# Kernel optimization log

Hardware: AMD Instinct MI355X
Metric: run time of the kernel (lower is better)

Reference implementation:

```python
import jax, jax.numpy as jnp
import numpy as np

WEIGHT = 0.1  # HISCLoss weight


def _gram(X):
    # linear kernel (the module's 'rbf' branch computes X @ Y.T)
    X = X.reshape(X.shape[0], -1)
    return X @ X.T  # [B, B]


def _center(K):
    # H K H with H = I - 11^T/B  ==  K - rowmean - colmean + grandmean
    rm = K.mean(axis=1, keepdims=True)
    cm = K.mean(axis=0, keepdims=True)
    gm = K.mean()
    return K - rm - cm + gm


def _hsic(X, Y):
    B = X.shape[0]
    Kc = _center(_gram(X))
    Lc = _center(_gram(Y))
    # trace(Kc @ Lc) without the B^3 matmul
    tr = jnp.einsum('ij,ji->', Kc, Lc)
    return tr / ((B - 1) ** 2)


def setup_inputs() -> dict:
    key = jax.random.key(0)
    ks = jax.random.split(key, 4)
    B, d = 4096, 256
    return {
        'e0': jax.random.normal(ks[0], (B, d), dtype=jnp.float32),
        'e1': jax.random.normal(ks[1], (B, d), dtype=jnp.float32),
        'e2': jax.random.normal(ks[2], (B, d), dtype=jnp.float32),
        'e3': jax.random.normal(ks[3], (B, d), dtype=jnp.float32),
    }


def reference(e0, e1, e2, e3):
    experts = [e0, e1, e2, e3]
    n = len(experts)
    vals = []
    for i in range(n):
        for j in range(i + 1, n):
            vals.append(_hsic(experts[i], experts[j]))
    L_hsic = jnp.mean(jnp.stack(vals))
    return WEIGHT * L_hsic
```

## Files before the change

### kernel.cpp

```cpp
#include <hip/hip_runtime.h>
#include <hip/hip_bf16.h>

#define B_ROWS 4096
#define DIM 256
#define NPAIR 6
#define PITCH 4160
#define BK 256
#define APITCH 264
#define KSPLIT 8
#define KCHUNK (B_ROWS / KSPLIT)

typedef short bf16x8 __attribute__((ext_vector_type(8)));
typedef float f32x4 __attribute__((ext_vector_type(4)));

__device__ __forceinline__ const float* sel(const float* e0, const float* e1,
                                            const float* e2, const float* e3, int i) {
    return i == 0 ? e0 : (i == 1 ? e1 : (i == 2 ? e2 : e3));
}

__device__ __forceinline__ int pair_i(int p) { return p < 3 ? 0 : (p < 5 ? 1 : 2); }
__device__ __forceinline__ int pair_j(int p) { return p < 3 ? p + 1 : (p < 5 ? p - 1 : 3); }

__device__ __forceinline__ unsigned short f32_to_bf16_rne(float f) {
    unsigned int u = __float_as_uint(f);
    unsigned int r = (u + 0x7FFFu + ((u >> 16) & 1u)) >> 16;
    return (unsigned short)r;
}


__global__ __launch_bounds__(256) void transpose_bf16_kernel(
        const float* __restrict__ e0, const float* __restrict__ e1,
        const float* __restrict__ e2, const float* __restrict__ e3,
        unsigned short* __restrict__ XT, float* __restrict__ sums) {
    int rt = blockIdx.x;
    int ct = blockIdx.y;
    int e  = blockIdx.z;
    const float* X = sel(e0, e1, e2, e3, e);
    unsigned short* XTe = XT + (size_t)e * DIM * PITCH;

    __shared__ float T[64][65];

    int t = threadIdx.x;
    int c4 = (t & 15) << 2;
    #pragma unroll
    for (int p = 0; p < 4; ++p) {
        int r = (t >> 4) + 16 * p;
        float4 v = *(const float4*)&X[(size_t)(rt * 64 + r) * DIM + ct * 64 + c4];
        T[c4 + 0][r] = v.x;
        T[c4 + 1][r] = v.y;
        T[c4 + 2][r] = v.z;
        T[c4 + 3][r] = v.w;
    }
    __syncthreads();

    #pragma unroll
    for (int p = 0; p < 2; ++p) {
        int id = 256 * p + t;
        int c = id >> 3;
        int roff = (id & 7) * 8;
        bf16x8 outv;
        float s8 = 0.f;
        #pragma unroll
        for (int s = 0; s < 8; ++s) {
            float f = T[c][roff + s];
            outv[s] = (short)f32_to_bf16_rne(f);
            s8 += f;
        }
        *(bf16x8*)&XTe[(size_t)(ct * 64 + c) * PITCH + rt * 64 + roff] = outv;
        s8 += __shfl_down(s8, 4, 8);
        s8 += __shfl_down(s8, 2, 8);
        s8 += __shfl_down(s8, 1, 8);
        if ((id & 7) == 0) atomicAdd(&sums[e * DIM + ct * 64 + c], s8);
    }
}

__global__ __launch_bounds__(512) void gram_v3_kernel(
        const unsigned short* __restrict__ XT, const float* __restrict__ sums,
        float* __restrict__ acc_out) {
    __shared__ __align__(16) unsigned short smem[2 * 32 * APITCH];
    unsigned short* As = smem;
    unsigned short* Bs = smem + 32 * APITCH;
    float* red = (float*)smem;

    int blk = blockIdx.x;
    int p = blk >> 6;
    int tile = blk & 63;
    int a0 = (tile >> 3) * 32;
    int b0 = (tile & 7) * 32;
    int pi = pair_i(p), pj = pair_j(p);
    const unsigned short* Xp = XT + (size_t)pi * DIM * PITCH;
    const unsigned short* Yp = XT + (size_t)pj * DIM * PITCH;

    int tid = threadIdx.x;
    int w = tid >> 6;
    int L = tid & 63;

    int srow = tid >> 5;
    int soff = (tid & 31) * 8;
    const unsigned short* gA0 = Xp + (size_t)(a0 + srow) * PITCH + soff;
    const unsigned short* gA1 = Xp + (size_t)(a0 + 16 + srow) * PITCH + soff;
    const unsigned short* gB0 = Yp + (size_t)(b0 + srow) * PITCH + soff;
    const unsigned short* gB1 = Yp + (size_t)(b0 + 16 + srow) * PITCH + soff;
    int lA0 = srow * APITCH + soff;
    int lA1 = (16 + srow) * APITCH + soff;

    bf16x8 ra0 = *(const bf16x8*)gA0;
    bf16x8 ra1 = *(const bf16x8*)gA1;
    bf16x8 rb0 = *(const bf16x8*)gB0;
    bf16x8 rb1 = *(const bf16x8*)gB1;

    f32x4 acc[2][2] = {};
    int koff = w * 32 + (L >> 4) * 8;
    int frA0 = (L & 15) * APITCH + koff;
    int frA1 = (16 + (L & 15)) * APITCH + koff;

    for (int c = 0; c < 16; ++c) {
        __syncthreads();
        *(bf16x8*)&As[lA0] = ra0;
        *(bf16x8*)&As[lA1] = ra1;
        *(bf16x8*)&Bs[lA0] = rb0;
        *(bf16x8*)&Bs[lA1] = rb1;
        int cn = (c < 15) ? (c + 1) * BK : 0;
        ra0 = *(const bf16x8*)(gA0 + cn);
        ra1 = *(const bf16x8*)(gA1 + cn);
        rb0 = *(const bf16x8*)(gB0 + cn);
        rb1 = *(const bf16x8*)(gB1 + cn);
        __syncthreads();
        bf16x8 a0f = *(const bf16x8*)&As[frA0];
        bf16x8 a1f = *(const bf16x8*)&As[frA1];
        bf16x8 b0f = *(const bf16x8*)&Bs[frA0];
        bf16x8 b1f = *(const bf16x8*)&Bs[frA1];
        acc[0][0] = __builtin_amdgcn_mfma_f32_16x16x32_bf16(a0f, b0f, acc[0][0], 0, 0, 0);
        acc[0][1] = __builtin_amdgcn_mfma_f32_16x16x32_bf16(a0f, b1f, acc[0][1], 0, 0, 0);
        acc[1][0] = __builtin_amdgcn_mfma_f32_16x16x32_bf16(a1f, b0f, acc[1][0], 0, 0, 0);
        acc[1][1] = __builtin_amdgcn_mfma_f32_16x16x32_bf16(a1f, b1f, acc[1][1], 0, 0, 0);
    }

    __syncthreads();

    #pragma unroll
    for (int ti = 0; ti < 2; ++ti)
        #pragma unroll
        for (int tj = 0; tj < 2; ++tj)
            #pragma unroll
            for (int r = 0; r < 4; ++r) {
                int m = ti * 16 + (L >> 4) * 4 + r;
                int n = tj * 16 + (L & 15);
                red[w * 1056 + m * 33 + n] = acc[ti][tj][r];
            }
    __syncthreads();

    const float inv_b = 1.0f / (float)B_ROWS;
    float local = 0.f;
    #pragma unroll
    for (int q = 0; q < 2; ++q) {
        int pos = tid + q * 512;
        int m = pos >> 5, n = pos & 31;
        float s = 0.f;
        #pragma unroll
        for (int ww = 0; ww < 8; ++ww) s += red[ww * 1056 + m * 33 + n];
        float v = s - sums[pi * DIM + a0 + m] * sums[pj * DIM + b0 + n] * inv_b;
        local = fmaf(v, v, local);
    }
    #pragma unroll
    for (int off = 32; off > 0; off >>= 1) local += __shfl_down(local, off, 64);
    __shared__ float wsum[8];
    if (L == 0) wsum[w] = local;
    __syncthreads();
    if (tid == 0) {
        float s = 0.f;
        #pragma unroll
        for (int ww = 0; ww < 8; ++ww) s += wsum[ww];
        atomicAdd(acc_out, s);
    }
}

__global__ void finalize_kernel(const float* __restrict__ acc, float* __restrict__ out) {
    if (threadIdx.x == 0) {
        const float scale = 0.1f / (6.0f * 4095.0f * 4095.0f);
        out[0] = acc[0] * scale;
    }
}


__global__ void col_sums_kernel(const float* __restrict__ e0, const float* __restrict__ e1,
                                const float* __restrict__ e2, const float* __restrict__ e3,
                                float* __restrict__ sums) {
    int e = blockIdx.y;
    const float* X = sel(e0, e1, e2, e3, e);
    int c = threadIdx.x;
    int r0 = blockIdx.x * 128;
    float s = 0.f;
    #pragma unroll 4
    for (int r = r0; r < r0 + 128; ++r) s += X[r * DIM + c];
    atomicAdd(&sums[e * DIM + c], s);
}

__global__ __launch_bounds__(256) void gram_kernel(
        const float* __restrict__ e0, const float* __restrict__ e1,
        const float* __restrict__ e2, const float* __restrict__ e3,
        float* __restrict__ G) {
    int kc = blockIdx.x;
    int tile = blockIdx.y;
    int p = blockIdx.z;
    const float* X = sel(e0, e1, e2, e3, pair_i(p));
    const float* Y = sel(e0, e1, e2, e3, pair_j(p));
    int a0 = (tile >> 2) * 64;
    int b0 = (tile & 3) * 64;
    int k0 = kc * KCHUNK;
    __shared__ float As[16][64];
    __shared__ float Bs[16][64];
    int lid = threadIdx.x;
    int lr = lid >> 4;
    int lc = (lid & 15) << 2;
    int ty = lid >> 4;
    int tx = lid & 15;
    float acc[4][4] = {};
    for (int ks = 0; ks < KCHUNK; ks += 16) {
        int row = k0 + ks + lr;
        float4 av = *(const float4*)&X[row * DIM + a0 + lc];
        float4 bv = *(const float4*)&Y[row * DIM + b0 + lc];
        __syncthreads();
        *(float4*)&As[lr][lc] = av;
        *(float4*)&Bs[lr][lc] = bv;
        __syncthreads();
        #pragma unroll
        for (int k = 0; k < 16; ++k) {
            float a[4], b[4];
            *(float4*)a = *(const float4*)&As[k][ty * 4];
            *(float4*)b = *(const float4*)&Bs[k][tx * 4];
            #pragma unroll
            for (int i = 0; i < 4; ++i)
                #pragma unroll
                for (int j = 0; j < 4; ++j)
                    acc[i][j] = fmaf(a[i], b[j], acc[i][j]);
        }
    }
    float* Gp = G + p * (DIM * DIM);
    #pragma unroll
    for (int i = 0; i < 4; ++i)
        #pragma unroll
        for (int j = 0; j < 4; ++j)
            atomicAdd(&Gp[(a0 + ty * 4 + i) * DIM + (b0 + tx * 4 + j)], acc[i][j]);
}

__global__ void reduce_kernel(const float* __restrict__ G, const float* __restrict__ sums,
                              float* __restrict__ acc) {
    float local = 0.f;
    const int total = NPAIR * DIM * DIM;
    for (int idx = blockIdx.x * blockDim.x + threadIdx.x; idx < total;
         idx += gridDim.x * blockDim.x) {
        int p = idx >> 16;
        int ab = idx & 65535;
        int a = ab >> 8;
        int b = ab & 255;
        float v = G[idx] - sums[pair_i(p) * DIM + a] * sums[pair_j(p) * DIM + b] * (1.0f / (float)B_ROWS);
        local = fmaf(v, v, local);
    }
    #pragma unroll
    for (int off = 32; off > 0; off >>= 1) local += __shfl_down(local, off, 64);
    __shared__ float wsum[4];
    if ((threadIdx.x & 63) == 0) wsum[threadIdx.x >> 6] = local;
    __syncthreads();
    if (threadIdx.x == 0) {
        float s = wsum[0] + wsum[1] + wsum[2] + wsum[3];
        atomicAdd(acc, s);
    }
}


extern "C" void kernel_launch(void* const* d_in, const int* in_sizes, int n_in,
                              void* d_out, int out_size, void* d_ws, size_t ws_size,
                              hipStream_t stream) {
    const float* e0 = (const float*)d_in[0];
    const float* e1 = (const float*)d_in[1];
    const float* e2 = (const float*)d_in[2];
    const float* e3 = (const float*)d_in[3];

    float* sums = (float*)d_ws;
    float* acc  = (float*)((char*)d_ws + 4096);
    size_t need = 8192 + (size_t)4 * DIM * PITCH * sizeof(unsigned short);

    if (ws_size >= need) {
        unsigned short* XT = (unsigned short*)((char*)d_ws + 8192);
        hipMemsetAsync(d_ws, 0, 8192, stream);
        transpose_bf16_kernel<<<dim3(64, 4, 4), 256, 0, stream>>>(e0, e1, e2, e3, XT, sums);
        gram_v3_kernel<<<NPAIR * 64, 512, 0, stream>>>(XT, sums, acc);
        finalize_kernel<<<1, 64, 0, stream>>>(acc, (float*)d_out);
    } else {
        float* G = (float*)((char*)d_ws + 8192);
        size_t zbytes = 8192 + (size_t)NPAIR * DIM * DIM * sizeof(float);
        hipMemsetAsync(d_ws, 0, zbytes, stream);
        col_sums_kernel<<<dim3(32, 4), 256, 0, stream>>>(e0, e1, e2, e3, sums);
        gram_kernel<<<dim3(KSPLIT, 16, NPAIR), 256, 0, stream>>>(e0, e1, e2, e3, G);
        reduce_kernel<<<384, 256, 0, stream>>>(G, sums, acc);
        finalize_kernel<<<1, 64, 0, stream>>>(acc, (float*)d_out);
    }
}
```

Before: 91.52 us.

## Load MFMA fragments directly from global memory with per-wave K split

The gram kernel drops its LDS staging and block barriers. Each wave now owns a contiguous 512-element K range and loads its bf16 fragments straight from global memory into registers, prefetching the next chunk while the MFMAs run. Block indices are also swizzled so that adjacent blocks are spread across pairs and tiles, which changes L2 locality across XCDs. The trade-off is less coalesced global access per wave, in exchange for removing the barriers and LDS traffic.

```diff
diff --git a/kernel.cpp b/kernel.cpp
--- a/kernel.cpp
+++ b/kernel.cpp
@@ -5,8 +5,6 @@
 #define DIM 256
 #define NPAIR 6
 #define PITCH 4160
-#define BK 256
-#define APITCH 264
 #define KSPLIT 8
 #define KCHUNK (B_ROWS / KSPLIT)
 
@@ -74,17 +72,16 @@
     }
 }
 
-__global__ __launch_bounds__(512) void gram_v3_kernel(
+__global__ __launch_bounds__(512) void gram_v4_kernel(
         const unsigned short* __restrict__ XT, const float* __restrict__ sums,
         float* __restrict__ acc_out) {
-    __shared__ __align__(16) unsigned short smem[2 * 32 * APITCH];
-    unsigned short* As = smem;
-    unsigned short* Bs = smem + 32 * APITCH;
-    float* red = (float*)smem;
+    __shared__ __align__(16) float red[8 * 1056];
+    __shared__ float wsum[8];
 
     int blk = blockIdx.x;
-    int p = blk >> 6;
-    int tile = blk & 63;
+    int swz = (blk & 7) * 48 + (blk >> 3);
+    int p = swz >> 6;
+    int tile = swz & 63;
     int a0 = (tile >> 3) * 32;
     int b0 = (tile & 7) * 32;
     int pi = pair_i(p), pj = pair_j(p);
@@ -95,48 +92,32 @@
     int w = tid >> 6;
     int L = tid & 63;
 
-    int srow = tid >> 5;
-    int soff = (tid & 31) * 8;
-    const unsigned short* gA0 = Xp + (size_t)(a0 + srow) * PITCH + soff;
-    const unsigned short* gA1 = Xp + (size_t)(a0 + 16 + srow) * PITCH + soff;
-    const unsigned short* gB0 = Yp + (size_t)(b0 + srow) * PITCH + soff;
-    const unsigned short* gB1 = Yp + (size_t)(b0 + 16 + srow) * PITCH + soff;
-    int lA0 = srow * APITCH + soff;
-    int lA1 = (16 + srow) * APITCH + soff;
-
-    bf16x8 ra0 = *(const bf16x8*)gA0;
-    bf16x8 ra1 = *(const bf16x8*)gA1;
-    bf16x8 rb0 = *(const bf16x8*)gB0;
-    bf16x8 rb1 = *(const bf16x8*)gB1;
+    int kbase = w * 512 + (L >> 4) * 8;
+    const unsigned short* pA0 = Xp + (size_t)(a0 + (L & 15)) * PITCH + kbase;
+    const unsigned short* pA1 = pA0 + (size_t)16 * PITCH;
+    const unsigned short* pB0 = Yp + (size_t)(b0 + (L & 15)) * PITCH + kbase;
+    const unsigned short* pB1 = pB0 + (size_t)16 * PITCH;
 
     f32x4 acc[2][2] = {};
-    int koff = w * 32 + (L >> 4) * 8;
-    int frA0 = (L & 15) * APITCH + koff;
-    int frA1 = (16 + (L & 15)) * APITCH + koff;
-
+
+    bf16x8 a0f = *(const bf16x8*)pA0;
+    bf16x8 a1f = *(const bf16x8*)pA1;
+    bf16x8 b0f = *(const bf16x8*)pB0;
+    bf16x8 b1f = *(const bf16x8*)pB1;
+
+    #pragma unroll
     for (int c = 0; c < 16; ++c) {
-        __syncthreads();
-        *(bf16x8*)&As[lA0] = ra0;
-        *(bf16x8*)&As[lA1] = ra1;
-        *(bf16x8*)&Bs[lA0] = rb0;
-        *(bf16x8*)&Bs[lA1] = rb1;
-        int cn = (c < 15) ? (c + 1) * BK : 0;
-        ra0 = *(const bf16x8*)(gA0 + cn);
-        ra1 = *(const bf16x8*)(gA1 + cn);
-        rb0 = *(const bf16x8*)(gB0 + cn);
-        rb1 = *(const bf16x8*)(gB1 + cn);
-        __syncthreads();
-        bf16x8 a0f = *(const bf16x8*)&As[frA0];
-        bf16x8 a1f = *(const bf16x8*)&As[frA1];
-        bf16x8 b0f = *(const bf16x8*)&Bs[frA0];
-        bf16x8 b1f = *(const bf16x8*)&Bs[frA1];
+        int off = (c < 15) ? (c + 1) * 32 : 0;
+        bf16x8 na0 = *(const bf16x8*)(pA0 + off);
+        bf16x8 na1 = *(const bf16x8*)(pA1 + off);
+        bf16x8 nb0 = *(const bf16x8*)(pB0 + off);
+        bf16x8 nb1 = *(const bf16x8*)(pB1 + off);
         acc[0][0] = __builtin_amdgcn_mfma_f32_16x16x32_bf16(a0f, b0f, acc[0][0], 0, 0, 0);
         acc[0][1] = __builtin_amdgcn_mfma_f32_16x16x32_bf16(a0f, b1f, acc[0][1], 0, 0, 0);
         acc[1][0] = __builtin_amdgcn_mfma_f32_16x16x32_bf16(a1f, b0f, acc[1][0], 0, 0, 0);
         acc[1][1] = __builtin_amdgcn_mfma_f32_16x16x32_bf16(a1f, b1f, acc[1][1], 0, 0, 0);
-    }
-
-    __syncthreads();
+        a0f = na0; a1f = na1; b0f = nb0; b1f = nb1;
+    }
 
     #pragma unroll
     for (int ti = 0; ti < 2; ++ti)
@@ -164,7 +145,6 @@
     }
     #pragma unroll
     for (int off = 32; off > 0; off >>= 1) local += __shfl_down(local, off, 64);
-    __shared__ float wsum[8];
     if (L == 0) wsum[w] = local;
     __syncthreads();
     if (tid == 0) {
@@ -285,7 +265,7 @@
         unsigned short* XT = (unsigned short*)((char*)d_ws + 8192);
         hipMemsetAsync(d_ws, 0, 8192, stream);
         transpose_bf16_kernel<<<dim3(64, 4, 4), 256, 0, stream>>>(e0, e1, e2, e3, XT, sums);
-        gram_v3_kernel<<<NPAIR * 64, 512, 0, stream>>>(XT, sums, acc);
+        gram_v4_kernel<<<NPAIR * 64, 512, 0, stream>>>(XT, sums, acc);
         finalize_kernel<<<1, 64, 0, stream>>>(acc, (float*)d_out);
     } else {
         float* G = (float*)((char*)d_ws + 8192);
```

After: 106.6 us. 16.4% more time.

## Double-buffer LDS in gram kernel, swizzle blocks, fuse finalize via last-block counter

Applied to the files above, without the earlier changes.

Gives the gram kernel two LDS stages so the next K chunk is written while the current one feeds the MFMAs. This cuts the per-iteration barriers from two to one. Block indices are remapped so neighbouring blocks spread across pairs and tiles. The separate finalize launch is removed: a global counter lets the last block write the scaled result. The cost is twice the shared memory, which may lower occupancy, and added atomics and fences.

```diff
diff --git a/kernel.cpp b/kernel.cpp
--- a/kernel.cpp
+++ b/kernel.cpp
@@ -74,17 +74,17 @@
     }
 }
 
-__global__ __launch_bounds__(512) void gram_v3_kernel(
+__global__ __launch_bounds__(512) void gram_v5_kernel(
         const unsigned short* __restrict__ XT, const float* __restrict__ sums,
-        float* __restrict__ acc_out) {
-    __shared__ __align__(16) unsigned short smem[2 * 32 * APITCH];
-    unsigned short* As = smem;
-    unsigned short* Bs = smem + 32 * APITCH;
-    float* red = (float*)smem;
+        float* __restrict__ acc_out, unsigned int* __restrict__ cnt,
+        float* __restrict__ out) {
+    __shared__ __align__(16) unsigned short smem[2 * 64 * APITCH];
+    __shared__ float wsum[8];
 
     int blk = blockIdx.x;
-    int p = blk >> 6;
-    int tile = blk & 63;
+    int swz = (blk & 7) * 48 + (blk >> 3);
+    int p = swz >> 6;
+    int tile = swz & 63;
     int a0 = (tile >> 3) * 32;
     int b0 = (tile & 7) * 32;
     int pi = pair_i(p), pj = pair_j(p);
@@ -104,39 +104,57 @@
     int lA0 = srow * APITCH + soff;
     int lA1 = (16 + srow) * APITCH + soff;
 
+    f32x4 acc[2][2] = {};
+    int koff = w * 32 + (L >> 4) * 8;
+    int frA0 = (L & 15) * APITCH + koff;
+    int frA1 = (16 + (L & 15)) * APITCH + koff;
+
     bf16x8 ra0 = *(const bf16x8*)gA0;
     bf16x8 ra1 = *(const bf16x8*)gA1;
     bf16x8 rb0 = *(const bf16x8*)gB0;
     bf16x8 rb1 = *(const bf16x8*)gB1;
 
-    f32x4 acc[2][2] = {};
-    int koff = w * 32 + (L >> 4) * 8;
-    int frA0 = (L & 15) * APITCH + koff;
-    int frA1 = (16 + (L & 15)) * APITCH + koff;
-
+    #define STAGE(buf) do {                                             \
+        unsigned short* As_ = smem + (buf) * (64 * APITCH);             \
+        unsigned short* Bs_ = As_ + 32 * APITCH;                        \
+        *(bf16x8*)&As_[lA0] = ra0;                                      \
+        *(bf16x8*)&As_[lA1] = ra1;                                      \
+        *(bf16x8*)&Bs_[lA0] = rb0;                                      \
+        *(bf16x8*)&Bs_[lA1] = rb1;                                      \
+    } while (0)
+
+    STAGE(0);
+    ra0 = *(const bf16x8*)(gA0 + BK);
+    ra1 = *(const bf16x8*)(gA1 + BK);
+    rb0 = *(const bf16x8*)(gB0 + BK);
+    rb1 = *(const bf16x8*)(gB1 + BK);
+    __syncthreads();
+
+    #pragma unroll 2
     for (int c = 0; c < 16; ++c) {
-        __syncthreads();
-        *(bf16x8*)&As[lA0] = ra0;
-        *(bf16x8*)&As[lA1] = ra1;
-        *(bf16x8*)&Bs[lA0] = rb0;
-        *(bf16x8*)&Bs[lA1] = rb1;
-        int cn = (c < 15) ? (c + 1) * BK : 0;
-        ra0 = *(const bf16x8*)(gA0 + cn);
-        ra1 = *(const bf16x8*)(gA1 + cn);
-        rb0 = *(const bf16x8*)(gB0 + cn);
-        rb1 = *(const bf16x8*)(gB1 + cn);
-        __syncthreads();
-        bf16x8 a0f = *(const bf16x8*)&As[frA0];
-        bf16x8 a1f = *(const bf16x8*)&As[frA1];
-        bf16x8 b0f = *(const bf16x8*)&Bs[frA0];
-        bf16x8 b1f = *(const bf16x8*)&Bs[frA1];
+        const unsigned short* As_ = smem + (c & 1) * (64 * APITCH);
+        const unsigned short* Bs_ = As_ + 32 * APITCH;
+        bf16x8 a0f = *(const bf16x8*)&As_[frA0];
+        bf16x8 a1f = *(const bf16x8*)&As_[frA1];
+        bf16x8 b0f = *(const bf16x8*)&Bs_[frA0];
+        bf16x8 b1f = *(const bf16x8*)&Bs_[frA1];
+        if (c < 15) {
+            STAGE((c + 1) & 1);
+            int cn = (c < 14) ? (c + 2) * BK : 0;
+            ra0 = *(const bf16x8*)(gA0 + cn);
+            ra1 = *(const bf16x8*)(gA1 + cn);
+            rb0 = *(const bf16x8*)(gB0 + cn);
+            rb1 = *(const bf16x8*)(gB1 + cn);
+        }
         acc[0][0] = __builtin_amdgcn_mfma_f32_16x16x32_bf16(a0f, b0f, acc[0][0], 0, 0, 0);
         acc[0][1] = __builtin_amdgcn_mfma_f32_16x16x32_bf16(a0f, b1f, acc[0][1], 0, 0, 0);
         acc[1][0] = __builtin_amdgcn_mfma_f32_16x16x32_bf16(a1f, b0f, acc[1][0], 0, 0, 0);
         acc[1][1] = __builtin_amdgcn_mfma_f32_16x16x32_bf16(a1f, b1f, acc[1][1], 0, 0, 0);
-    }
-
-    __syncthreads();
+        __syncthreads();
+    }
+    #undef STAGE
+
+    float* red = (float*)smem;
 
     #pragma unroll
     for (int ti = 0; ti < 2; ++ti)
@@ -164,7 +182,6 @@
     }
     #pragma unroll
     for (int off = 32; off > 0; off >>= 1) local += __shfl_down(local, off, 64);
-    __shared__ float wsum[8];
     if (L == 0) wsum[w] = local;
     __syncthreads();
     if (tid == 0) {
@@ -172,6 +189,13 @@
         #pragma unroll
         for (int ww = 0; ww < 8; ++ww) s += wsum[ww];
         atomicAdd(acc_out, s);
+        __threadfence();
+        unsigned int old = atomicAdd(cnt, 1u);
+        if (old == (unsigned int)(gridDim.x - 1)) {
+            float tot = atomicAdd(acc_out, 0.0f);
+            const float scale = 0.1f / (6.0f * 4095.0f * 4095.0f);
+            out[0] = tot * scale;
+        }
     }
 }
 
@@ -279,14 +303,14 @@
 
     float* sums = (float*)d_ws;
     float* acc  = (float*)((char*)d_ws + 4096);
+    unsigned int* cnt = (unsigned int*)((char*)d_ws + 4096 + 4);
     size_t need = 8192 + (size_t)4 * DIM * PITCH * sizeof(unsigned short);
 
     if (ws_size >= need) {
         unsigned short* XT = (unsigned short*)((char*)d_ws + 8192);
         hipMemsetAsync(d_ws, 0, 8192, stream);
         transpose_bf16_kernel<<<dim3(64, 4, 4), 256, 0, stream>>>(e0, e1, e2, e3, XT, sums);
-        gram_v3_kernel<<<NPAIR * 64, 512, 0, stream>>>(XT, sums, acc);
-        finalize_kernel<<<1, 64, 0, stream>>>(acc, (float*)d_out);
+        gram_v5_kernel<<<NPAIR * 64, 512, 0, stream>>>(XT, sums, acc, cnt, (float*)d_out);
     } else {
         float* G = (float*)((char*)d_ws + 8192);
         size_t zbytes = 8192 + (size_t)NPAIR * DIM * DIM * sizeof(float);
```

After: 97.01 us. 1.06x slower.

## Halve gram tile width to double block count and fuse finalize via last-block counter

Applied to the files above, without the earlier changes.

The gram kernel now computes 32x16 output tiles instead of 32x32, which doubles the grid from 384 to 768 blocks so more of the GPU's compute units are occupied. Each block also halves its B loads and MFMA work. The separate finalize kernel is removed: the last block to finish, found with an atomic counter and a threadfence, scales and writes the output, saving one launch. In exchange, the A tile is loaded from global memory twice as often across the grid, and every block does one more atomic.

```diff
diff --git a/kernel.cpp b/kernel.cpp
--- a/kernel.cpp
+++ b/kernel.cpp
@@ -74,19 +74,20 @@
     }
 }
 
-__global__ __launch_bounds__(512) void gram_v3_kernel(
+__global__ __launch_bounds__(512) void gram_v6_kernel(
         const unsigned short* __restrict__ XT, const float* __restrict__ sums,
-        float* __restrict__ acc_out) {
-    __shared__ __align__(16) unsigned short smem[2 * 32 * APITCH];
+        float* __restrict__ acc_out, unsigned int* __restrict__ cnt,
+        float* __restrict__ out) {
+    __shared__ __align__(16) unsigned short smem[48 * APITCH];
+    __shared__ float wsum[8];
     unsigned short* As = smem;
     unsigned short* Bs = smem + 32 * APITCH;
-    float* red = (float*)smem;
 
     int blk = blockIdx.x;
-    int p = blk >> 6;
-    int tile = blk & 63;
-    int a0 = (tile >> 3) * 32;
-    int b0 = (tile & 7) * 32;
+    int p = blk >> 7;
+    int tile = blk & 127;
+    int a0 = (tile >> 4) * 32;
+    int b0 = (tile & 15) * 16;
     int pi = pair_i(p), pj = pair_j(p);
     const unsigned short* Xp = XT + (size_t)pi * DIM * PITCH;
     const unsigned short* Yp = XT + (size_t)pj * DIM * PITCH;
@@ -100,16 +101,14 @@
     const unsigned short* gA0 = Xp + (size_t)(a0 + srow) * PITCH + soff;
     const unsigned short* gA1 = Xp + (size_t)(a0 + 16 + srow) * PITCH + soff;
     const unsigned short* gB0 = Yp + (size_t)(b0 + srow) * PITCH + soff;
-    const unsigned short* gB1 = Yp + (size_t)(b0 + 16 + srow) * PITCH + soff;
     int lA0 = srow * APITCH + soff;
     int lA1 = (16 + srow) * APITCH + soff;
 
     bf16x8 ra0 = *(const bf16x8*)gA0;
     bf16x8 ra1 = *(const bf16x8*)gA1;
     bf16x8 rb0 = *(const bf16x8*)gB0;
-    bf16x8 rb1 = *(const bf16x8*)gB1;
-
-    f32x4 acc[2][2] = {};
+
+    f32x4 acc[2] = {};
     int koff = w * 32 + (L >> 4) * 8;
     int frA0 = (L & 15) * APITCH + koff;
     int frA1 = (16 + (L & 15)) * APITCH + koff;
@@ -119,59 +118,55 @@
         *(bf16x8*)&As[lA0] = ra0;
         *(bf16x8*)&As[lA1] = ra1;
         *(bf16x8*)&Bs[lA0] = rb0;
-        *(bf16x8*)&Bs[lA1] = rb1;
         int cn = (c < 15) ? (c + 1) * BK : 0;
         ra0 = *(const bf16x8*)(gA0 + cn);
         ra1 = *(const bf16x8*)(gA1 + cn);
         rb0 = *(const bf16x8*)(gB0 + cn);
-        rb1 = *(const bf16x8*)(gB1 + cn);
         __syncthreads();
         bf16x8 a0f = *(const bf16x8*)&As[frA0];
         bf16x8 a1f = *(const bf16x8*)&As[frA1];
         bf16x8 b0f = *(const bf16x8*)&Bs[frA0];
-        bf16x8 b1f = *(const bf16x8*)&Bs[frA1];
-        acc[0][0] = __builtin_amdgcn_mfma_f32_16x16x32_bf16(a0f, b0f, acc[0][0], 0, 0, 0);
-        acc[0][1] = __builtin_amdgcn_mfma_f32_16x16x32_bf16(a0f, b1f, acc[0][1], 0, 0, 0);
-        acc[1][0] = __builtin_amdgcn_mfma_f32_16x16x32_bf16(a1f, b0f, acc[1][0], 0, 0, 0);
-        acc[1][1] = __builtin_amdgcn_mfma_f32_16x16x32_bf16(a1f, b1f, acc[1][1], 0, 0, 0);
-    }
-
-    __syncthreads();
+        acc[0] = __builtin_amdgcn_mfma_f32_16x16x32_bf16(a0f, b0f, acc[0], 0, 0, 0);
+        acc[1] = __builtin_amdgcn_mfma_f32_16x16x32_bf16(a1f, b0f, acc[1], 0, 0, 0);
+    }
+
+    __syncthreads();
+
+    float* red = (float*)smem;
 
     #pragma unroll
     for (int ti = 0; ti < 2; ++ti)
         #pragma unroll
-        for (int tj = 0; tj < 2; ++tj)
-            #pragma unroll
-            for (int r = 0; r < 4; ++r) {
-                int m = ti * 16 + (L >> 4) * 4 + r;
-                int n = tj * 16 + (L & 15);
-                red[w * 1056 + m * 33 + n] = acc[ti][tj][r];
-            }
+        for (int r = 0; r < 4; ++r) {
+            int m = ti * 16 + (L >> 4) * 4 + r;
+            int n = L & 15;
+            red[w * 544 + m * 17 + n] = acc[ti][r];
+        }
     __syncthreads();
 
     const float inv_b = 1.0f / (float)B_ROWS;
-    float local = 0.f;
-    #pragma unroll
-    for (int q = 0; q < 2; ++q) {
-        int pos = tid + q * 512;
-        int m = pos >> 5, n = pos & 31;
-        float s = 0.f;
-        #pragma unroll
-        for (int ww = 0; ww < 8; ++ww) s += red[ww * 1056 + m * 33 + n];
-        float v = s - sums[pi * DIM + a0 + m] * sums[pj * DIM + b0 + n] * inv_b;
-        local = fmaf(v, v, local);
-    }
+    int m = tid >> 4, n = tid & 15;
+    float s = 0.f;
+    #pragma unroll
+    for (int ww = 0; ww < 8; ++ww) s += red[ww * 544 + m * 17 + n];
+    float v = s - sums[pi * DIM + a0 + m] * sums[pj * DIM + b0 + n] * inv_b;
+    float local = v * v;
     #pragma unroll
     for (int off = 32; off > 0; off >>= 1) local += __shfl_down(local, off, 64);
-    __shared__ float wsum[8];
     if (L == 0) wsum[w] = local;
     __syncthreads();
     if (tid == 0) {
-        float s = 0.f;
-        #pragma unroll
-        for (int ww = 0; ww < 8; ++ww) s += wsum[ww];
-        atomicAdd(acc_out, s);
+        float s2 = 0.f;
+        #pragma unroll
+        for (int ww = 0; ww < 8; ++ww) s2 += wsum[ww];
+        atomicAdd(acc_out, s2);
+        __threadfence();
+        unsigned int old = atomicAdd(cnt, 1u);
+        if (old == (unsigned int)(gridDim.x - 1)) {
+            float tot = atomicAdd(acc_out, 0.0f);
+            const float scale = 0.1f / (6.0f * 4095.0f * 4095.0f);
+            out[0] = tot * scale;
+        }
     }
 }
 
@@ -279,14 +274,14 @@
 
     float* sums = (float*)d_ws;
     float* acc  = (float*)((char*)d_ws + 4096);
+    unsigned int* cnt = (unsigned int*)((char*)d_ws + 4096 + 4);
     size_t need = 8192 + (size_t)4 * DIM * PITCH * sizeof(unsigned short);
 
     if (ws_size >= need) {
         unsigned short* XT = (unsigned short*)((char*)d_ws + 8192);
         hipMemsetAsync(d_ws, 0, 8192, stream);
         transpose_bf16_kernel<<<dim3(64, 4, 4), 256, 0, stream>>>(e0, e1, e2, e3, XT, sums);
-        gram_v3_kernel<<<NPAIR * 64, 512, 0, stream>>>(XT, sums, acc);
-        finalize_kernel<<<1, 64, 0, stream>>>(acc, (float*)d_out);
+        gram_v6_kernel<<<NPAIR * 128, 512, 0, stream>>>(XT, sums, acc, cnt, (float*)d_out);
     } else {
         float* G = (float*)((char*)d_ws + 8192);
         size_t zbytes = 8192 + (size_t)NPAIR * DIM * DIM * sizeof(float);
```

Measured after the change: 108.9 us. 1.19x slower.
